# Performance work log

Hardware: AMD Instinct MI355X
Metric: run time of the kernel (lower is better)

## Reference

```python
import jax, jax.numpy as jnp
import numpy as np

D_MODEL = 1024
N_HEADS = 16
D_K = D_MODEL // N_HEADS
NEG_INF = -1.0e9


def setup_inputs() -> dict:
    key = jax.random.key(0)
    ks = jax.random.split(key, 12)
    B, S = 2, 2048
    inp = {
        "q": jax.random.normal(ks[0], (B, S, D_MODEL), dtype=jnp.float32),
        "k": jax.random.normal(ks[1], (B, S, D_MODEL), dtype=jnp.float32),
        "v": jax.random.normal(ks[2], (B, S, D_MODEL), dtype=jnp.float32),
        "mask": jax.random.randint(ks[3], (B, 1, S, S), 0, 2, dtype=jnp.int32),
        "Wq": jax.random.normal(ks[4], (D_MODEL, D_MODEL), dtype=jnp.float32) / np.sqrt(D_MODEL),
        "bq": jnp.zeros((D_MODEL,), dtype=jnp.float32),
        "Wk": jax.random.normal(ks[5], (D_MODEL, D_MODEL), dtype=jnp.float32) / np.sqrt(D_MODEL),
        "bk": jnp.zeros((D_MODEL,), dtype=jnp.float32),
        "Wv": jax.random.normal(ks[6], (D_MODEL, D_MODEL), dtype=jnp.float32) / np.sqrt(D_MODEL),
        "bv": jnp.zeros((D_MODEL,), dtype=jnp.float32),
        "Wo": jax.random.normal(ks[7], (D_MODEL, D_MODEL), dtype=jnp.float32) / np.sqrt(D_MODEL),
        "bo": jnp.zeros((D_MODEL,), dtype=jnp.float32),
    }
    return inp


def _split_heads(x):
    B, S, _ = x.shape
    return x.reshape(B, S, N_HEADS, D_K).transpose(0, 2, 1, 3)  # [B,H,S,Dk]


def reference(q, k, v, mask, Wq, bq, Wk, bk, Wv, bv, Wo, bo):
    # QKV projections (nn.Linear: x @ W.T + b; here W stored as [in,out]-agnostic square)
    query = _split_heads(q @ Wq + bq)
    key_ = _split_heads(k @ Wk + bk)
    value = _split_heads(v @ Wv + bv)

    scale = 1.0 / np.sqrt(D_K).astype(np.float32)
    scores = jnp.einsum("bhqd,bhkd->bhqk", query, key_) * scale  # [B,H,S,S]
    scores = jnp.where(mask == 0, NEG_INF, scores)
    attn = jax.nn.softmax(scores, axis=-1)  # dropout is identity in eval (p=0.0)
    ctx = jnp.einsum("bhqk,bhkd->bhqd", attn, value)  # [B,H,S,Dk]

    B, H, S, Dk = ctx.shape
    ctx = ctx.transpose(0, 2, 1, 3).reshape(B, S, H * Dk)
    return ctx @ Wo + bo
```

## Files before the change

kernel.cpp:

```cpp
#include <hip/hip_runtime.h>
#include <hip/hip_bf16.h>

typedef __bf16 bf16_t;
typedef __bf16 bf16x2 __attribute__((ext_vector_type(2)));
typedef __bf16 bf16x8 __attribute__((ext_vector_type(8)));
typedef float f32x4 __attribute__((ext_vector_type(4)));
typedef float f32x16 __attribute__((ext_vector_type(16)));
typedef int intx4 __attribute__((ext_vector_type(4)));
typedef unsigned int u32;
typedef unsigned long long u64;

#define S_LEN 2048
#define DM 1024
#define NH 16
#define DK 64
#define M_ROWS 4096
#define SCALE_LOG2E 0.1803368801111204f

__device__ __forceinline__ int sw_off(int row, int col) {
  return row * 64 + ((((col >> 3) ^ row) & 7) << 3) + (col & 7);
}

__device__ __forceinline__ bf16x8 cvt8(const float4& a, const float4& b) {
  bf16x8 v;
  v[0] = (__bf16)a.x; v[1] = (__bf16)a.y; v[2] = (__bf16)a.z; v[3] = (__bf16)a.w;
  v[4] = (__bf16)b.x; v[5] = (__bf16)b.y; v[6] = (__bf16)b.z; v[7] = (__bf16)b.w;
  return v;
}

__device__ __forceinline__ void glds16(const bf16_t* g, bf16_t* l) {
  __builtin_amdgcn_global_load_lds(
      (const __attribute__((address_space(1))) void*)g,
      (__attribute__((address_space(3))) void*)l, 16, 0, 0);
}

__device__ __forceinline__ int pk2(float lo, float hi) {
  bf16x2 t;
  t[0] = (__bf16)lo;
  t[1] = (__bf16)hi;
  return __builtin_bit_cast(int, t);
}

__global__ __launch_bounds__(256) void pack_mask(
    const int* __restrict__ mask, u64* __restrict__ mb)
{
  const int wgl = blockIdx.x * 4 + (threadIdx.x >> 6);
  const int lane = threadIdx.x & 63;
  const int q = wgl & 2047;
  const int kw = (wgl >> 11) & 31;
  const int b = wgl >> 16;
  const int val = mask[((size_t)(b * S_LEN + q)) * S_LEN + kw * 64 + lane];
  const u64 bits = __ballot(val != 0);
  if (lane == 0) mb[wgl] = bits;
}

__global__ __launch_bounds__(256) void cvt_inputs(
    const float* __restrict__ q, const float* __restrict__ k,
    const float* __restrict__ v, bf16_t* __restrict__ Xb)
{
  const int z = blockIdx.y;
  const float* __restrict__ src = (z == 0) ? q : ((z == 1) ? k : v);
  const size_t idx = ((size_t)blockIdx.x * 256 + threadIdx.x) * 8;
  const float4 a = *(const float4*)&src[idx];
  const float4 b = *(const float4*)&src[idx + 4];
  *(bf16x8*)&Xb[(size_t)z * M_ROWS * DM + idx] = cvt8(a, b);
}

__global__ __launch_bounds__(256) void transw_kernel(
    const float* __restrict__ Wq, const float* __restrict__ Wk,
    const float* __restrict__ Wv, const float* __restrict__ Wo,
    bf16_t* __restrict__ Wt)
{
  const int z = blockIdx.z;
  const float* __restrict__ W = (z == 0) ? Wq : ((z == 1) ? Wk : ((z == 2) ? Wv : Wo));
  bf16_t* __restrict__ out = Wt + (size_t)z * DM * DM;
  __shared__ float tile[64][65];
  const int tx = threadIdx.x & 31, ty = threadIdx.x >> 5;
  const int k0 = blockIdx.x * 64, n0 = blockIdx.y * 64;
  #pragma unroll
  for (int j = 0; j < 8; ++j) {
    const float2 v = *(const float2*)&W[(size_t)(k0 + ty + 8 * j) * DM + n0 + tx * 2];
    tile[ty + 8 * j][tx * 2] = v.x;
    tile[ty + 8 * j][tx * 2 + 1] = v.y;
  }
  __syncthreads();
  #pragma unroll
  for (int j = 0; j < 8; ++j) {
    const int a = ty + 8 * j;
    bf16x2 p;
    p[0] = (__bf16)tile[tx * 2][a];
    p[1] = (__bf16)tile[tx * 2 + 1][a];
    *(bf16x2*)&out[(size_t)(n0 + a) * DM + k0 + tx * 2] = p;
  }
}

__device__ __forceinline__ void gemm128_body(
    const bf16_t* __restrict__ A, const bf16_t* __restrict__ Bt,
    const float* __restrict__ bias, bf16_t* __restrict__ outb,
    float* __restrict__ outf)
{
  __shared__ __align__(16) bf16_t As[128 * 32];
  __shared__ __align__(16) bf16_t Bs[128 * 32];
  const int t = threadIdx.x, w = t >> 6, L = t & 63, quad = L >> 4, l16 = L & 15;
  const int m0 = blockIdx.x * 128, n0 = blockIdx.y * 128;
  const int mb = 64 * (w & 1), nb = 64 * (w >> 1);
  const int rowS = t >> 2, subS = (t & 3) * 8;

  f32x4 acc[4][4] = {};
  for (int k0 = 0; k0 < DM; k0 += 32) {
    __syncthreads();
    glds16(&A[(size_t)(m0 + rowS) * DM + k0 + subS],        &As[t * 8]);
    glds16(&A[(size_t)(m0 + 64 + rowS) * DM + k0 + subS],   &As[2048 + t * 8]);
    glds16(&Bt[(size_t)(n0 + rowS) * DM + k0 + subS],       &Bs[t * 8]);
    glds16(&Bt[(size_t)(n0 + 64 + rowS) * DM + k0 + subS],  &Bs[2048 + t * 8]);
    __syncthreads();
    bf16x8 af[4], bfr[4];
    #pragma unroll
    for (int mt = 0; mt < 4; ++mt)
      af[mt] = *(const bf16x8*)&As[(mb + 16 * mt + l16) * 32 + quad * 8];
    #pragma unroll
    for (int ct = 0; ct < 4; ++ct)
      bfr[ct] = *(const bf16x8*)&Bs[(nb + 16 * ct + l16) * 32 + quad * 8];
    #pragma unroll
    for (int mt = 0; mt < 4; ++mt)
      #pragma unroll
      for (int ct = 0; ct < 4; ++ct)
        acc[mt][ct] = __builtin_amdgcn_mfma_f32_16x16x32_bf16(af[mt], bfr[ct], acc[mt][ct], 0, 0, 0);
  }
  #pragma unroll
  for (int mt = 0; mt < 4; ++mt)
    #pragma unroll
    for (int ct = 0; ct < 4; ++ct)
      #pragma unroll
      for (int r = 0; r < 4; ++r) {
        const int row = m0 + mb + 16 * mt + quad * 4 + r;
        const int n = n0 + nb + 16 * ct + l16;
        const float val = acc[mt][ct][r] + bias[n];
        if (outb) outb[(size_t)row * DM + n] = (__bf16)val;
        else      outf[(size_t)row * DM + n] = val;
      }
}

__global__ __launch_bounds__(256) void gemm_qkv(
    const bf16_t* __restrict__ Xb, const bf16_t* __restrict__ Wt,
    const float* __restrict__ bq, const float* __restrict__ bk,
    const float* __restrict__ bv, bf16_t* __restrict__ QKVb)
{
  const int z = blockIdx.z;
  gemm128_body(Xb + (size_t)z * M_ROWS * DM, Wt + (size_t)z * DM * DM,
               (z == 0) ? bq : ((z == 1) ? bk : bv),
               QKVb + (size_t)z * M_ROWS * DM, nullptr);
}

__global__ __launch_bounds__(256) void gemm_out(
    const bf16_t* __restrict__ ctx, const bf16_t* __restrict__ Wto,
    const float* __restrict__ bo, float* __restrict__ out)
{
  gemm128_body(ctx, Wto, bo, nullptr, out);
}

__global__ __launch_bounds__(256) void transpV(
    const bf16_t* __restrict__ Vb, bf16_t* __restrict__ Vtw)
{
  __shared__ bf16_t Tr[64 * 72];
  const int t = threadIdx.x;
  const int key0 = blockIdx.x * 64;
  const int bh = blockIdx.y, b = bh >> 4, h = bh & 15;
  const int r = t >> 2, c = (t & 3) * 16;
  const bf16_t* src = &Vb[(size_t)(b * S_LEN + key0 + r) * DM + h * DK + c];
  const bf16x8 v0 = *(const bf16x8*)src;
  const bf16x8 v1 = *(const bf16x8*)(src + 8);
  #pragma unroll
  for (int j = 0; j < 8; ++j) {
    Tr[r * 72 + c + j] = v0[j];
    Tr[r * 72 + c + 8 + j] = v1[j];
  }
  __syncthreads();
  const int dv = t >> 2, kc = (t & 3) * 16;
  bf16_t ov[16];
  #pragma unroll
  for (int j = 0; j < 16; ++j) ov[j] = Tr[(kc + j) * 72 + dv];
  bf16_t* dst = &Vtw[((size_t)bh * DK + dv) * S_LEN + key0 + kc];
  *(bf16x8*)dst = *(bf16x8*)&ov[0];
  *(bf16x8*)(dst + 8) = *(bf16x8*)&ov[8];
}

__global__ __launch_bounds__(256, 2) void attn_kernel(
    const bf16_t* __restrict__ Qb, const bf16_t* __restrict__ Kb,
    const bf16_t* __restrict__ Vtw, const u64* __restrict__ mb,
    bf16_t* __restrict__ ctx)
{
  __shared__ __align__(16) bf16_t Qs[128 * 64];
  __shared__ __align__(16) bf16_t Ks[2][64 * 64];
  __shared__ __align__(16) bf16_t Vts[2][64 * 64];

  const int t = threadIdx.x, w = t >> 6, L = t & 63;
  const int l31 = L & 31, h5 = L >> 5;
  const int q0 = blockIdx.x * 128;
  const int bh = blockIdx.y, b = bh >> 4, h = bh & 15;
  const int sr = t >> 2, sc = (t & 3) * 16;

  #pragma unroll
  for (int half = 0; half < 2; ++half) {
    const int row = half * 64 + sr;
    const bf16_t* s = &Qb[(size_t)(b * S_LEN + q0 + row) * DM + h * DK + sc];
    *(bf16x8*)&Qs[sw_off(row, sc)]     = *(const bf16x8*)s;
    *(bf16x8*)&Qs[sw_off(row, sc + 8)] = *(const bf16x8*)(s + 8);
  }
  __syncthreads();

  bf16x8 qf[4];
  #pragma unroll
  for (int ks = 0; ks < 4; ++ks)
    qf[ks] = *(const bf16x8*)&Qs[sw_off(32 * w + l31, ks * 16 + 8 * h5)];

  const int ch = (L & 7) ^ (L >> 3);
  const int row0 = w * 16 + (L >> 3);
  const int kofs0 = w * 1024 + L * 8, kofs1 = kofs0 + 512;
  const bf16_t* pK0 = &Kb[(size_t)(b * S_LEN + row0) * DM + h * DK + ch * 8];
  const bf16_t* pK1 = pK0 + (size_t)8 * DM;
  const bf16_t* pV0 = &Vtw[((size_t)bh * DK + row0) * S_LEN + ch * 8];
  const bf16_t* pV1 = pV0 + (size_t)8 * S_LEN;

  const int qg = q0 + 32 * w + l31;
  const u64* pm = &mb[(size_t)b * 32 * S_LEN + qg];

  auto stageKV = [&](int buf) {
    glds16(pK0, &Ks[buf][kofs0]);
    glds16(pK1, &Ks[buf][kofs1]);
    glds16(pV0, &Vts[buf][kofs0]);
    glds16(pV1, &Vts[buf][kofs1]);
    pK0 += (size_t)64 * DM; pK1 += (size_t)64 * DM;
    pV0 += 64; pV1 += 64;
  };

  f32x16 O[2] = {};
  float l_lane = 0.f;

  auto compute = [&](const bf16_t* __restrict__ Kc, const bf16_t* __restrict__ Vc,
                     u64 mcur) {
    f32x16 sacc[2] = {};
    __builtin_amdgcn_s_setprio(1);
    #pragma unroll
    for (int ks = 0; ks < 4; ++ks)
      #pragma unroll
      for (int nt = 0; nt < 2; ++nt) {
        const bf16x8 kf = *(const bf16x8*)&Kc[sw_off(nt * 32 + l31, ks * 16 + 8 * h5)];
        sacc[nt] = __builtin_amdgcn_mfma_f32_32x32x16_bf16(kf, qf[ks], sacc[nt], 0, 0, 0);
      }
    __builtin_amdgcn_s_setprio(0);
    const u32 mlo = ((u32)mcur) >> (4 * h5);
    const u32 mhi = ((u32)(mcur >> 32)) >> (4 * h5);
    #pragma unroll
    for (int nt = 0; nt < 2; ++nt) {
      const u32 mm = nt ? mhi : mlo;
      float p[16];
      #pragma unroll
      for (int r = 0; r < 16; ++r) {
        const int cb = (r & 3) + 8 * (r >> 2);
        float v = __builtin_exp2f(__builtin_fmaf(sacc[nt][r], SCALE_LOG2E, -16.f));
        v = ((mm >> cb) & 1u) ? v : 0.f;
        l_lane += v;
        p[r] = v;
      }
      #pragma unroll
      for (int ss = 0; ss < 2; ++ss) {
        const int x0 = pk2(p[8 * ss + 0], p[8 * ss + 1]);
        const int x1 = pk2(p[8 * ss + 2], p[8 * ss + 3]);
        const int y0 = pk2(p[8 * ss + 4], p[8 * ss + 5]);
        const int y1 = pk2(p[8 * ss + 6], p[8 * ss + 7]);
        const auto r0 = __builtin_amdgcn_permlane32_swap(x0, y0, false, false);
        const auto r1 = __builtin_amdgcn_permlane32_swap(x1, y1, false, false);
        intx4 wv;
        wv[0] = r0[0]; wv[1] = r1[0]; wv[2] = r0[1]; wv[3] = r1[1];
        const bf16x8 pf = __builtin_bit_cast(bf16x8, wv);
        const int s4 = 2 * nt + ss;
        __builtin_amdgcn_s_setprio(1);
        #pragma unroll
        for (int ot = 0; ot < 2; ++ot) {
          const bf16x8 vf = *(const bf16x8*)&Vc[sw_off(32 * ot + l31, s4 * 16 + 8 * h5)];
          O[ot] = __builtin_amdgcn_mfma_f32_32x32x16_bf16(vf, pf, O[ot], 0, 0, 0);
        }
        __builtin_amdgcn_s_setprio(0);
      }
    }
  };

  stageKV(0);
  u64 mcur = *pm; pm += S_LEN;
  u64 mnext;
  __syncthreads();

  for (int kt = 0; kt < S_LEN / 64; kt += 2) {
    stageKV(1);
    mnext = *pm; pm += S_LEN;
    compute(&Ks[0][0], &Vts[0][0], mcur);
    __syncthreads();
    mcur = mnext;
    if (kt + 2 < S_LEN / 64) {
      stageKV(0);
      mnext = *pm; pm += S_LEN;
    }
    compute(&Ks[1][0], &Vts[1][0], mcur);
    __syncthreads();
    mcur = mnext;
  }

  const float lsum = l_lane + __shfl_xor(l_lane, 32);
  const float inv = 1.f / lsum;
  #pragma unroll
  for (int ot = 0; ot < 2; ++ot)
    #pragma unroll
    for (int r = 0; r < 16; ++r) {
      const int dv = 32 * ot + (r & 3) + 8 * (r >> 2) + 4 * h5;
      Qs[sw_off(32 * w + l31, dv)] = (__bf16)(O[ot][r] * inv);
    }
  const int erow = 32 * w + (L >> 1);
  const int ecol = (L & 1) * 32;
  bf16_t* dst = &ctx[(size_t)(b * S_LEN + q0 + erow) * DM + h * DK + ecol];
  #pragma unroll
  for (int c8 = 0; c8 < 4; ++c8)
    *(bf16x8*)(dst + 8 * c8) = *(const bf16x8*)&Qs[sw_off(erow, ecol + 8 * c8)];
}

extern "C" void kernel_launch(void* const* d_in, const int* in_sizes, int n_in,
                              void* d_out, int out_size, void* d_ws, size_t ws_size,
                              hipStream_t stream) {
  const float* q  = (const float*)d_in[0];
  const float* k  = (const float*)d_in[1];
  const float* v  = (const float*)d_in[2];
  const int* mask = (const int*)d_in[3];
  const float* Wq = (const float*)d_in[4];
  const float* bq = (const float*)d_in[5];
  const float* Wk = (const float*)d_in[6];
  const float* bk = (const float*)d_in[7];
  const float* Wv = (const float*)d_in[8];
  const float* bv = (const float*)d_in[9];
  const float* Wo = (const float*)d_in[10];
  const float* bo = (const float*)d_in[11];
  float* out = (float*)d_out;

  const size_t SLICE = (size_t)M_ROWS * DM;
  bf16_t* Xb   = (bf16_t*)d_ws;
  bf16_t* QKVb = Xb + 3 * SLICE;
  bf16_t* Wt   = QKVb + 3 * SLICE;
  u64* mbw     = (u64*)(Wt + (size_t)4 * DM * DM);
  bf16_t* ctx  = Xb;
  bf16_t* Vtw  = Xb + SLICE;

  pack_mask<<<dim3(32768), dim3(256), 0, stream>>>(mask, mbw);
  cvt_inputs<<<dim3(2048, 3), dim3(256), 0, stream>>>(q, k, v, Xb);
  transw_kernel<<<dim3(16, 16, 4), dim3(256), 0, stream>>>(Wq, Wk, Wv, Wo, Wt);
  gemm_qkv<<<dim3(32, 8, 3), dim3(256), 0, stream>>>(Xb, Wt, bq, bk, bv, QKVb);
  transpV<<<dim3(32, 32), dim3(256), 0, stream>>>(QKVb + 2 * SLICE, Vtw);
  attn_kernel<<<dim3(16, 32), dim3(256), 0, stream>>>(QKVb, QKVb + SLICE, Vtw, mbw, ctx);
  gemm_out<<<dim3(32, 8), dim3(256), 0, stream>>>(ctx, Wt + (size_t)3 * DM * DM, bo, out);
}
```

Measured before the change: 286.8 us.

## Split key tiles across wave pairs in attention to double block count

Halves the query rows per attention block and assigns wave pairs to the two 32-key halves of each tile, merging partial outputs and row sums through shared memory at the end. The grid doubles and launch bounds allow four blocks per CU, aiming to raise occupancy and latency hiding. In exchange, each K/V tile is fetched by twice as many blocks, MFMA work per loaded tile halves, and there is an extra reduction and barrier at the end.

```diff
diff --git a/kernel.cpp b/kernel.cpp
--- a/kernel.cpp
+++ b/kernel.cpp
@@ -185,34 +185,32 @@
   *(bf16x8*)(dst + 8) = *(bf16x8*)&ov[8];
 }
 
-__global__ __launch_bounds__(256, 2) void attn_kernel(
+__global__ __launch_bounds__(256, 4) void attn_kernel(
     const bf16_t* __restrict__ Qb, const bf16_t* __restrict__ Kb,
     const bf16_t* __restrict__ Vtw, const u64* __restrict__ mb,
     bf16_t* __restrict__ ctx)
 {
-  __shared__ __align__(16) bf16_t Qs[128 * 64];
-  __shared__ __align__(16) bf16_t Ks[2][64 * 64];
-  __shared__ __align__(16) bf16_t Vts[2][64 * 64];
+  __shared__ __align__(16) bf16_t Qs[64 * 64];
+  __shared__ __align__(16) bf16_t KVs[4][64 * 64];
 
   const int t = threadIdx.x, w = t >> 6, L = t & 63;
   const int l31 = L & 31, h5 = L >> 5;
-  const int q0 = blockIdx.x * 128;
+  const int qhalf = w & 1, khalf = w >> 1;
+  const int q0 = blockIdx.x * 64;
   const int bh = blockIdx.y, b = bh >> 4, h = bh & 15;
   const int sr = t >> 2, sc = (t & 3) * 16;
 
-  #pragma unroll
-  for (int half = 0; half < 2; ++half) {
-    const int row = half * 64 + sr;
-    const bf16_t* s = &Qb[(size_t)(b * S_LEN + q0 + row) * DM + h * DK + sc];
-    *(bf16x8*)&Qs[sw_off(row, sc)]     = *(const bf16x8*)s;
-    *(bf16x8*)&Qs[sw_off(row, sc + 8)] = *(const bf16x8*)(s + 8);
+  {
+    const bf16_t* s = &Qb[(size_t)(b * S_LEN + q0 + sr) * DM + h * DK + sc];
+    *(bf16x8*)&Qs[sw_off(sr, sc)]     = *(const bf16x8*)s;
+    *(bf16x8*)&Qs[sw_off(sr, sc + 8)] = *(const bf16x8*)(s + 8);
   }
   __syncthreads();
 
   bf16x8 qf[4];
   #pragma unroll
   for (int ks = 0; ks < 4; ++ks)
-    qf[ks] = *(const bf16x8*)&Qs[sw_off(32 * w + l31, ks * 16 + 8 * h5)];
+    qf[ks] = *(const bf16x8*)&Qs[sw_off(32 * qhalf + l31, ks * 16 + 8 * h5)];
 
   const int ch = (L & 7) ^ (L >> 3);
   const int row0 = w * 16 + (L >> 3);
@@ -222,14 +220,14 @@
   const bf16_t* pV0 = &Vtw[((size_t)bh * DK + row0) * S_LEN + ch * 8];
   const bf16_t* pV1 = pV0 + (size_t)8 * S_LEN;
 
-  const int qg = q0 + 32 * w + l31;
+  const int qg = q0 + 32 * qhalf + l31;
   const u64* pm = &mb[(size_t)b * 32 * S_LEN + qg];
 
   auto stageKV = [&](int buf) {
-    glds16(pK0, &Ks[buf][kofs0]);
-    glds16(pK1, &Ks[buf][kofs1]);
-    glds16(pV0, &Vts[buf][kofs0]);
-    glds16(pV1, &Vts[buf][kofs1]);
+    glds16(pK0, &KVs[buf][kofs0]);
+    glds16(pK1, &KVs[buf][kofs1]);
+    glds16(pV0, &KVs[2 + buf][kofs0]);
+    glds16(pV1, &KVs[2 + buf][kofs1]);
     pK0 += (size_t)64 * DM; pK1 += (size_t)64 * DM;
     pV0 += 64; pV1 += 64;
   };
@@ -237,52 +235,46 @@
   f32x16 O[2] = {};
   float l_lane = 0.f;
 
-  auto compute = [&](const bf16_t* __restrict__ Kc, const bf16_t* __restrict__ Vc,
-                     u64 mcur) {
-    f32x16 sacc[2] = {};
+  auto compute = [&](int buf, u64 mcur) {
+    const bf16_t* __restrict__ Kc = &KVs[buf][0];
+    const bf16_t* __restrict__ Vc = &KVs[2 + buf][0];
+    f32x16 sacc = {};
     __builtin_amdgcn_s_setprio(1);
     #pragma unroll
-    for (int ks = 0; ks < 4; ++ks)
-      #pragma unroll
-      for (int nt = 0; nt < 2; ++nt) {
-        const bf16x8 kf = *(const bf16x8*)&Kc[sw_off(nt * 32 + l31, ks * 16 + 8 * h5)];
-        sacc[nt] = __builtin_amdgcn_mfma_f32_32x32x16_bf16(kf, qf[ks], sacc[nt], 0, 0, 0);
+    for (int ks = 0; ks < 4; ++ks) {
+      const bf16x8 kf = *(const bf16x8*)&Kc[sw_off(khalf * 32 + l31, ks * 16 + 8 * h5)];
+      sacc = __builtin_amdgcn_mfma_f32_32x32x16_bf16(kf, qf[ks], sacc, 0, 0, 0);
+    }
+    __builtin_amdgcn_s_setprio(0);
+    const u32 mm = ((u32)(mcur >> (khalf ? 32 : 0))) >> (4 * h5);
+    float p[16];
+    #pragma unroll
+    for (int r = 0; r < 16; ++r) {
+      const int cb = (r & 3) + 8 * (r >> 2);
+      float v = __builtin_exp2f(__builtin_fmaf(sacc[r], SCALE_LOG2E, -16.f));
+      v = ((mm >> cb) & 1u) ? v : 0.f;
+      l_lane += v;
+      p[r] = v;
+    }
+    #pragma unroll
+    for (int ss = 0; ss < 2; ++ss) {
+      const int x0 = pk2(p[8 * ss + 0], p[8 * ss + 1]);
+      const int x1 = pk2(p[8 * ss + 2], p[8 * ss + 3]);
+      const int y0 = pk2(p[8 * ss + 4], p[8 * ss + 5]);
+      const int y1 = pk2(p[8 * ss + 6], p[8 * ss + 7]);
+      const auto r0 = __builtin_amdgcn_permlane32_swap(x0, y0, false, false);
+      const auto r1 = __builtin_amdgcn_permlane32_swap(x1, y1, false, false);
+      intx4 wv;
+      wv[0] = r0[0]; wv[1] = r1[0]; wv[2] = r0[1]; wv[3] = r1[1];
+      const bf16x8 pf = __builtin_bit_cast(bf16x8, wv);
+      const int s4 = 2 * khalf + ss;
+      __builtin_amdgcn_s_setprio(1);
+      #pragma unroll
+      for (int ot = 0; ot < 2; ++ot) {
+        const bf16x8 vf = *(const bf16x8*)&Vc[sw_off(32 * ot + l31, s4 * 16 + 8 * h5)];
+        O[ot] = __builtin_amdgcn_mfma_f32_32x32x16_bf16(vf, pf, O[ot], 0, 0, 0);
       }
-    __builtin_amdgcn_s_setprio(0);
-    const u32 mlo = ((u32)mcur) >> (4 * h5);
-    const u32 mhi = ((u32)(mcur >> 32)) >> (4 * h5);
-    #pragma unroll
-    for (int nt = 0; nt < 2; ++nt) {
-      const u32 mm = nt ? mhi : mlo;
-      float p[16];
-      #pragma unroll
-      for (int r = 0; r < 16; ++r) {
-        const int cb = (r & 3) + 8 * (r >> 2);
-        float v = __builtin_exp2f(__builtin_fmaf(sacc[nt][r], SCALE_LOG2E, -16.f));
-        v = ((mm >> cb) & 1u) ? v : 0.f;
-        l_lane += v;
-        p[r] = v;
-      }
-      #pragma unroll
-      for (int ss = 0; ss < 2; ++ss) {
-        const int x0 = pk2(p[8 * ss + 0], p[8 * ss + 1]);
-        const int x1 = pk2(p[8 * ss + 2], p[8 * ss + 3]);
-        const int y0 = pk2(p[8 * ss + 4], p[8 * ss + 5]);
-        const int y1 = pk2(p[8 * ss + 6], p[8 * ss + 7]);
-        const auto r0 = __builtin_amdgcn_permlane32_swap(x0, y0, false, false);
-        const auto r1 = __builtin_amdgcn_permlane32_swap(x1, y1, false, false);
-        intx4 wv;
-        wv[0] = r0[0]; wv[1] = r1[0]; wv[2] = r0[1]; wv[3] = r1[1];
-        const bf16x8 pf = __builtin_bit_cast(bf16x8, wv);
-        const int s4 = 2 * nt + ss;
-        __builtin_amdgcn_s_setprio(1);
-        #pragma unroll
-        for (int ot = 0; ot < 2; ++ot) {
-          const bf16x8 vf = *(const bf16x8*)&Vc[sw_off(32 * ot + l31, s4 * 16 + 8 * h5)];
-          O[ot] = __builtin_amdgcn_mfma_f32_32x32x16_bf16(vf, pf, O[ot], 0, 0, 0);
-        }
-        __builtin_amdgcn_s_setprio(0);
-      }
+      __builtin_amdgcn_s_setprio(0);
     }
   };
 
@@ -294,33 +286,49 @@
   for (int kt = 0; kt < S_LEN / 64; kt += 2) {
     stageKV(1);
     mnext = *pm; pm += S_LEN;
-    compute(&Ks[0][0], &Vts[0][0], mcur);
+    compute(0, mcur);
     __syncthreads();
     mcur = mnext;
     if (kt + 2 < S_LEN / 64) {
       stageKV(0);
       mnext = *pm; pm += S_LEN;
     }
-    compute(&Ks[1][0], &Vts[1][0], mcur);
+    compute(1, mcur);
     __syncthreads();
     mcur = mnext;
   }
 
-  const float lsum = l_lane + __shfl_xor(l_lane, 32);
-  const float inv = 1.f / lsum;
-  #pragma unroll
-  for (int ot = 0; ot < 2; ++ot)
-    #pragma unroll
-    for (int r = 0; r < 16; ++r) {
-      const int dv = 32 * ot + (r & 3) + 8 * (r >> 2) + 4 * h5;
-      Qs[sw_off(32 * w + l31, dv)] = (__bf16)(O[ot][r] * inv);
-    }
-  const int erow = 32 * w + (L >> 1);
-  const int ecol = (L & 1) * 32;
-  bf16_t* dst = &ctx[(size_t)(b * S_LEN + q0 + erow) * DM + h * DK + ecol];
-  #pragma unroll
-  for (int c8 = 0; c8 < 4; ++c8)
-    *(bf16x8*)(dst + 8 * c8) = *(const bf16x8*)&Qs[sw_off(erow, ecol + 8 * c8)];
+  const float lw = l_lane + __shfl_xor(l_lane, 32);
+  float* Osc = (float*)&KVs[0][0];
+  float* Lsc = Osc + 4096;
+  if (khalf == 1) {
+    #pragma unroll
+    for (int ot = 0; ot < 2; ++ot)
+      #pragma unroll
+      for (int r = 0; r < 16; ++r) {
+        const int dv = 32 * ot + (r & 3) + 8 * (r >> 2) + 4 * h5;
+        Osc[qhalf * 2048 + dv * 32 + l31] = O[ot][r];
+      }
+    if (h5 == 0) Lsc[qhalf * 32 + l31] = lw;
+  }
+  __syncthreads();
+  if (khalf == 0) {
+    const float inv = 1.f / (lw + Lsc[qhalf * 32 + l31]);
+    #pragma unroll
+    for (int ot = 0; ot < 2; ++ot)
+      #pragma unroll
+      for (int r = 0; r < 16; ++r) {
+        const int dv = 32 * ot + (r & 3) + 8 * (r >> 2) + 4 * h5;
+        const float val = (O[ot][r] + Osc[qhalf * 2048 + dv * 32 + l31]) * inv;
+        Qs[sw_off(32 * qhalf + l31, dv)] = (__bf16)val;
+      }
+    const int erow = 32 * qhalf + (L >> 1);
+    const int ecol = (L & 1) * 32;
+    bf16_t* dst = &ctx[(size_t)(b * S_LEN + q0 + erow) * DM + h * DK + ecol];
+    #pragma unroll
+    for (int c8 = 0; c8 < 4; ++c8)
+      *(bf16x8*)(dst + 8 * c8) = *(const bf16x8*)&Qs[sw_off(erow, ecol + 8 * c8)];
+  }
 }
 
 extern "C" void kernel_launch(void* const* d_in, const int* in_sizes, int n_in,
@@ -353,6 +361,6 @@
   transw_kernel<<<dim3(16, 16, 4), dim3(256), 0, stream>>>(Wq, Wk, Wv, Wo, Wt);
   gemm_qkv<<<dim3(32, 8, 3), dim3(256), 0, stream>>>(Xb, Wt, bq, bk, bv, QKVb);
   transpV<<<dim3(32, 32), dim3(256), 0, stream>>>(QKVb + 2 * SLICE, Vtw);
-  attn_kernel<<<dim3(16, 32), dim3(256), 0, stream>>>(QKVb, QKVb + SLICE, Vtw, mbw, ctx);
+  attn_kernel<<<dim3(32, 32), dim3(256), 0, stream>>>(QKVb, QKVb + SLICE, Vtw, mbw, ctx);
   gemm_out<<<dim3(32, 8), dim3(256), 0, stream>>>(ctx, Wt + (size_t)3 * DM * DM, bo, out);
 }
```

New measurement: 291.3 us. Within noise of the previous version (+1.6%).

## Fold softmax scale into Q projection and drop Q shared-memory staging

Applied to the files above, without the earlier changes.

The softmax scale times log2(e) is now applied in the Q projection epilogue, so the attention inner loop calls exp2 directly on the scores and loses the per-element FMA and its -16 offset. Q fragments are loaded straight from global memory into registers instead of being staged through a 16KB shared buffer with a block barrier. That cuts attention LDS use from 48KB to 32KB, and the output epilogue reuses each warp's slice of the K/V buffers. The mask select becomes a bitwise AND with a sign-extended bit. Without the -16 offset and with no running max, large scores are more likely to overflow, and the direct global Q loads are less coalesced.

```diff
diff --git a/kernel.cpp b/kernel.cpp
--- a/kernel.cpp
+++ b/kernel.cpp
@@ -96,8 +96,8 @@
 
 __device__ __forceinline__ void gemm128_body(
     const bf16_t* __restrict__ A, const bf16_t* __restrict__ Bt,
-    const float* __restrict__ bias, bf16_t* __restrict__ outb,
-    float* __restrict__ outf)
+    const float* __restrict__ bias, const float scale,
+    bf16_t* __restrict__ outb, float* __restrict__ outf)
 {
   __shared__ __align__(16) bf16_t As[128 * 32];
   __shared__ __align__(16) bf16_t Bs[128 * 32];
@@ -135,7 +135,7 @@
       for (int r = 0; r < 4; ++r) {
         const int row = m0 + mb + 16 * mt + quad * 4 + r;
         const int n = n0 + nb + 16 * ct + l16;
-        const float val = acc[mt][ct][r] + bias[n];
+        const float val = (acc[mt][ct][r] + bias[n]) * scale;
         if (outb) outb[(size_t)row * DM + n] = (__bf16)val;
         else      outf[(size_t)row * DM + n] = val;
       }
@@ -149,6 +149,7 @@
   const int z = blockIdx.z;
   gemm128_body(Xb + (size_t)z * M_ROWS * DM, Wt + (size_t)z * DM * DM,
                (z == 0) ? bq : ((z == 1) ? bk : bv),
+               (z == 0) ? SCALE_LOG2E : 1.0f,
                QKVb + (size_t)z * M_ROWS * DM, nullptr);
 }
 
@@ -156,7 +157,7 @@
     const bf16_t* __restrict__ ctx, const bf16_t* __restrict__ Wto,
     const float* __restrict__ bo, float* __restrict__ out)
 {
-  gemm128_body(ctx, Wto, bo, nullptr, out);
+  gemm128_body(ctx, Wto, bo, 1.0f, nullptr, out);
 }
 
 __global__ __launch_bounds__(256) void transpV(
@@ -190,46 +191,36 @@
     const bf16_t* __restrict__ Vtw, const u64* __restrict__ mb,
     bf16_t* __restrict__ ctx)
 {
-  __shared__ __align__(16) bf16_t Qs[128 * 64];
-  __shared__ __align__(16) bf16_t Ks[2][64 * 64];
-  __shared__ __align__(16) bf16_t Vts[2][64 * 64];
+  __shared__ __align__(16) bf16_t KVs[2][2][64 * 64];
 
   const int t = threadIdx.x, w = t >> 6, L = t & 63;
   const int l31 = L & 31, h5 = L >> 5;
   const int q0 = blockIdx.x * 128;
   const int bh = blockIdx.y, b = bh >> 4, h = bh & 15;
-  const int sr = t >> 2, sc = (t & 3) * 16;
-
-  #pragma unroll
-  for (int half = 0; half < 2; ++half) {
-    const int row = half * 64 + sr;
-    const bf16_t* s = &Qb[(size_t)(b * S_LEN + q0 + row) * DM + h * DK + sc];
-    *(bf16x8*)&Qs[sw_off(row, sc)]     = *(const bf16x8*)s;
-    *(bf16x8*)&Qs[sw_off(row, sc + 8)] = *(const bf16x8*)(s + 8);
-  }
-  __syncthreads();
 
   bf16x8 qf[4];
-  #pragma unroll
-  for (int ks = 0; ks < 4; ++ks)
-    qf[ks] = *(const bf16x8*)&Qs[sw_off(32 * w + l31, ks * 16 + 8 * h5)];
+  {
+    const bf16_t* qsrc =
+        &Qb[(size_t)(b * S_LEN + q0 + 32 * w + l31) * DM + h * DK + 8 * h5];
+    #pragma unroll
+    for (int ks = 0; ks < 4; ++ks) qf[ks] = *(const bf16x8*)(qsrc + 16 * ks);
+  }
 
   const int ch = (L & 7) ^ (L >> 3);
-  const int row0 = w * 16 + (L >> 3);
+  const int row0 = 16 * w + (L >> 3);
   const int kofs0 = w * 1024 + L * 8, kofs1 = kofs0 + 512;
   const bf16_t* pK0 = &Kb[(size_t)(b * S_LEN + row0) * DM + h * DK + ch * 8];
   const bf16_t* pK1 = pK0 + (size_t)8 * DM;
   const bf16_t* pV0 = &Vtw[((size_t)bh * DK + row0) * S_LEN + ch * 8];
   const bf16_t* pV1 = pV0 + (size_t)8 * S_LEN;
 
-  const int qg = q0 + 32 * w + l31;
-  const u64* pm = &mb[(size_t)b * 32 * S_LEN + qg];
+  const u64* pm = &mb[(size_t)b * 32 * S_LEN + q0 + 32 * w + l31];
 
   auto stageKV = [&](int buf) {
-    glds16(pK0, &Ks[buf][kofs0]);
-    glds16(pK1, &Ks[buf][kofs1]);
-    glds16(pV0, &Vts[buf][kofs0]);
-    glds16(pV1, &Vts[buf][kofs1]);
+    glds16(pK0, &KVs[buf][0][kofs0]);
+    glds16(pK1, &KVs[buf][0][kofs1]);
+    glds16(pV0, &KVs[buf][1][kofs0]);
+    glds16(pV1, &KVs[buf][1][kofs1]);
     pK0 += (size_t)64 * DM; pK1 += (size_t)64 * DM;
     pV0 += 64; pV1 += 64;
   };
@@ -237,31 +228,32 @@
   f32x16 O[2] = {};
   float l_lane = 0.f;
 
-  auto compute = [&](const bf16_t* __restrict__ Kc, const bf16_t* __restrict__ Vc,
-                     u64 mcur) {
-    f32x16 sacc[2] = {};
+  auto compute = [&](int buf, u64 mcur) {
+    const bf16_t* __restrict__ Kc = &KVs[buf][0][0];
+    const bf16_t* __restrict__ Vc = &KVs[buf][1][0];
+    f32x16 s0 = {}, s1 = {};
     __builtin_amdgcn_s_setprio(1);
     #pragma unroll
-    for (int ks = 0; ks < 4; ++ks)
-      #pragma unroll
-      for (int nt = 0; nt < 2; ++nt) {
-        const bf16x8 kf = *(const bf16x8*)&Kc[sw_off(nt * 32 + l31, ks * 16 + 8 * h5)];
-        sacc[nt] = __builtin_amdgcn_mfma_f32_32x32x16_bf16(kf, qf[ks], sacc[nt], 0, 0, 0);
-      }
+    for (int ks = 0; ks < 4; ++ks) {
+      const bf16x8 kf0 = *(const bf16x8*)&Kc[sw_off(l31, ks * 16 + 8 * h5)];
+      const bf16x8 kf1 = *(const bf16x8*)&Kc[sw_off(32 + l31, ks * 16 + 8 * h5)];
+      s0 = __builtin_amdgcn_mfma_f32_32x32x16_bf16(kf0, qf[ks], s0, 0, 0, 0);
+      s1 = __builtin_amdgcn_mfma_f32_32x32x16_bf16(kf1, qf[ks], s1, 0, 0, 0);
+    }
     __builtin_amdgcn_s_setprio(0);
-    const u32 mlo = ((u32)mcur) >> (4 * h5);
-    const u32 mhi = ((u32)(mcur >> 32)) >> (4 * h5);
     #pragma unroll
     for (int nt = 0; nt < 2; ++nt) {
-      const u32 mm = nt ? mhi : mlo;
+      const u32 mm = ((u32)(mcur >> (nt ? 32 : 0))) >> (4 * h5);
+      const f32x16 sacc = nt ? s1 : s0;
       float p[16];
       #pragma unroll
       for (int r = 0; r < 16; ++r) {
         const int cb = (r & 3) + 8 * (r >> 2);
-        float v = __builtin_exp2f(__builtin_fmaf(sacc[nt][r], SCALE_LOG2E, -16.f));
-        v = ((mm >> cb) & 1u) ? v : 0.f;
-        l_lane += v;
-        p[r] = v;
+        const u32 mr = (u32)(((int)(mm << (31 - cb))) >> 31);
+        const float e = __builtin_exp2f(sacc[r]);
+        const float pv = __builtin_bit_cast(float, __builtin_bit_cast(u32, e) & mr);
+        l_lane += pv;
+        p[r] = pv;
       }
       #pragma unroll
       for (int ss = 0; ss < 2; ++ss) {
@@ -275,12 +267,11 @@
         wv[0] = r0[0]; wv[1] = r1[0]; wv[2] = r0[1]; wv[3] = r1[1];
         const bf16x8 pf = __builtin_bit_cast(bf16x8, wv);
         const int s4 = 2 * nt + ss;
+        const bf16x8 vf0 = *(const bf16x8*)&Vc[sw_off(l31, s4 * 16 + 8 * h5)];
+        const bf16x8 vf1 = *(const bf16x8*)&Vc[sw_off(32 + l31, s4 * 16 + 8 * h5)];
         __builtin_amdgcn_s_setprio(1);
-        #pragma unroll
-        for (int ot = 0; ot < 2; ++ot) {
-          const bf16x8 vf = *(const bf16x8*)&Vc[sw_off(32 * ot + l31, s4 * 16 + 8 * h5)];
-          O[ot] = __builtin_amdgcn_mfma_f32_32x32x16_bf16(vf, pf, O[ot], 0, 0, 0);
-        }
+        O[0] = __builtin_amdgcn_mfma_f32_32x32x16_bf16(vf0, pf, O[0], 0, 0, 0);
+        O[1] = __builtin_amdgcn_mfma_f32_32x32x16_bf16(vf1, pf, O[1], 0, 0, 0);
         __builtin_amdgcn_s_setprio(0);
       }
     }
@@ -294,33 +285,33 @@
   for (int kt = 0; kt < S_LEN / 64; kt += 2) {
     stageKV(1);
     mnext = *pm; pm += S_LEN;
-    compute(&Ks[0][0], &Vts[0][0], mcur);
+    compute(0, mcur);
     __syncthreads();
     mcur = mnext;
     if (kt + 2 < S_LEN / 64) {
       stageKV(0);
       mnext = *pm; pm += S_LEN;
     }
-    compute(&Ks[1][0], &Vts[1][0], mcur);
+    compute(1, mcur);
     __syncthreads();
     mcur = mnext;
   }
 
   const float lsum = l_lane + __shfl_xor(l_lane, 32);
   const float inv = 1.f / lsum;
+  bf16_t* sc = &KVs[0][0][0] + (size_t)w * 2048;
   #pragma unroll
   for (int ot = 0; ot < 2; ++ot)
     #pragma unroll
     for (int r = 0; r < 16; ++r) {
       const int dv = 32 * ot + (r & 3) + 8 * (r >> 2) + 4 * h5;
-      Qs[sw_off(32 * w + l31, dv)] = (__bf16)(O[ot][r] * inv);
+      sc[sw_off(l31, dv)] = (__bf16)(O[ot][r] * inv);
     }
-  const int erow = 32 * w + (L >> 1);
-  const int ecol = (L & 1) * 32;
-  bf16_t* dst = &ctx[(size_t)(b * S_LEN + q0 + erow) * DM + h * DK + ecol];
+  const int erow = L >> 1, ecol = (L & 1) * 32;
+  bf16_t* dst = &ctx[(size_t)(b * S_LEN + q0 + 32 * w + erow) * DM + h * DK + ecol];
   #pragma unroll
   for (int c8 = 0; c8 < 4; ++c8)
-    *(bf16x8*)(dst + 8 * c8) = *(const bf16x8*)&Qs[sw_off(erow, ecol + 8 * c8)];
+    *(bf16x8*)(dst + 8 * c8) = *(const bf16x8*)&sc[sw_off(erow, ecol + 8 * c8)];
 }
 
 extern "C" void kernel_launch(void* const* d_in, const int* in_sizes, int n_in,
```

Result: faster. 280.2 us (-2.3%).
